# Kernel optimization log

Hardware: AMD Instinct MI355X
Metric: run time of the kernel (lower is better)

Reference implementation:

```python
import jax, jax.numpy as jnp
import numpy as np

OUT_H = OUT_W = 7
SCALE = 1.0 / 16.0
E = 256
HEADS = 8
DH = E // HEADS
ROI_GRID = 14          # scaled roi side (fixed by construction -> static shapes)
N_ROIS = 512
FH, FW = 152, 256
NQ = OUT_H * OUT_W     # 49 content queries
S = ROI_GRID * ROI_GRID  # 196 keys per roi


def setup_inputs() -> dict:
    key = jax.random.key(0)
    ks = jax.random.split(key, 8)
    features = jax.random.normal(ks[0], (1, E, FH, FW), jnp.float32)
    # rois [N,5] = (batch_idx, x1, y1, x2, y2) in image coords; side 224 px so
    # the rounded scaled grid is exactly 14x14 for every roi.
    side = ROI_GRID / SCALE  # 224.0
    x1 = jax.random.uniform(ks[1], (N_ROIS,), minval=0.0, maxval=FW / SCALE - side)
    y1 = jax.random.uniform(ks[2], (N_ROIS,), minval=0.0, maxval=FH / SCALE - side)
    rois = jnp.stack([jnp.zeros(N_ROIS), x1, y1, x1 + side, y1 + side], axis=1)
    content_queries = jax.random.normal(ks[3], (NQ, E), jnp.float32) * 0.02
    in_proj_weight = jax.random.normal(ks[4], (3 * E, E), jnp.float32) / np.sqrt(E)
    in_proj_bias = jnp.zeros((3 * E,), jnp.float32)
    out_proj_weight = jax.random.normal(ks[5], (E, E), jnp.float32) / np.sqrt(E)
    out_proj_bias = jnp.zeros((E,), jnp.float32)
    balance_param = jnp.asarray(0.0, jnp.float32)  # hardsigmoid -> 0.5
    return dict(features=features, rois=rois, content_queries=content_queries,
                in_proj_weight=in_proj_weight, in_proj_bias=in_proj_bias,
                out_proj_weight=out_proj_weight, out_proj_bias=out_proj_bias,
                balance_param=balance_param)


def _bilinear(fmap, y, x):
    """torchvision roi_align bilinear sampling. fmap [C,H,W]; y,x flat [S]."""
    C, H, W = fmap.shape
    valid = ((y >= -1.0) & (y <= H) & (x >= -1.0) & (x <= W)).astype(fmap.dtype)
    y = jnp.clip(y, 0.0, H - 1.0)
    x = jnp.clip(x, 0.0, W - 1.0)
    y0 = jnp.floor(y); x0 = jnp.floor(x)
    y0i = y0.astype(jnp.int32); x0i = x0.astype(jnp.int32)
    y1i = jnp.minimum(y0i + 1, H - 1); x1i = jnp.minimum(x0i + 1, W - 1)
    ly = y - y0; lx = x - x0; hy = 1.0 - ly; hx = 1.0 - lx
    f = lambda yi, xi: fmap[:, yi, xi]  # [C, S]
    val = (hy * hx) * f(y0i, x0i) + (hy * lx) * f(y0i, x1i) \
        + (ly * hx) * f(y1i, x0i) + (ly * lx) * f(y1i, x1i)
    return val * valid


def _roi_align(fmap, roi4, out_h, out_w, scale, sr):
    """aligned=True RoIAlign for one roi, static sampling ratio sr."""
    x1, y1, x2, y2 = roi4
    sx = x1 * scale - 0.5
    sy = y1 * scale - 0.5
    bw = (x2 - x1) * scale / out_w
    bh = (y2 - y1) * scale / out_h
    offs = (jnp.arange(sr, dtype=fmap.dtype) + 0.5) / sr
    ys = sy + (jnp.arange(out_h, dtype=fmap.dtype)[:, None] + offs[None, :]) * bh  # [out_h,sr]
    xs = sx + (jnp.arange(out_w, dtype=fmap.dtype)[:, None] + offs[None, :]) * bw  # [out_w,sr]
    Y = jnp.broadcast_to(ys[:, :, None, None], (out_h, sr, out_w, sr)).reshape(-1)
    X = jnp.broadcast_to(xs[None, None, :, :], (out_h, sr, out_w, sr)).reshape(-1)
    vals = _bilinear(fmap, Y, X)  # [C, out_h*sr*out_w*sr]
    C = fmap.shape[0]
    return vals.reshape(C, out_h, sr, out_w, sr).mean(axis=(2, 4))  # [C,out_h,out_w]


def reference(features, rois, content_queries, in_proj_weight, in_proj_bias,
              out_proj_weight, out_proj_bias, balance_param):
    fmap = features[0]                       # single image batch
    roi4 = rois[:, 1:]                       # boxes in image coords
    balance = jnp.clip(balance_param / 6.0 + 0.5, 0.0, 1.0)  # hardsigmoid(_balance)

    # position pool: RoIAlign(7x7, spatial_scale, sampling_ratio=-1 -> 2, aligned)
    pos = jax.vmap(lambda r: _roi_align(fmap, r, OUT_H, OUT_W, SCALE, 2))(roi4)
    pos = pos * balance                      # [N, C, 7, 7]

    # per-roi content pool on scaled rois at scale 1.0, grid 14x14, sr=1
    sroi = roi4 * SCALE
    cf = jax.vmap(lambda r: _roi_align(fmap, r, ROI_GRID, ROI_GRID, 1.0, 1))(sroi)
    cf = cf.reshape(N_ROIS, E, S).transpose(0, 2, 1)  # [N, S, E] (flatten(2).permute)

    # nn.MultiheadAttention(E, HEADS): shared queries, per-roi keys/values
    Wq, Wk, Wv = jnp.split(in_proj_weight, 3, axis=0)
    bq, bk, bv = jnp.split(in_proj_bias, 3, axis=0)
    q = (content_queries @ Wq.T + bq).reshape(NQ, HEADS, DH).transpose(1, 0, 2)  # [h,Q,d]
    k = (cf @ Wk.T + bk).reshape(N_ROIS, S, HEADS, DH)
    v = (cf @ Wv.T + bv).reshape(N_ROIS, S, HEADS, DH)
    logits = jnp.einsum('hqd,nshd->nhqs', q, k) / np.sqrt(DH).astype(np.float32)
    attn = jax.nn.softmax(logits, axis=-1)                     # [N,h,Q,S]
    o = jnp.einsum('nhqs,nshd->nqhd', attn, v).reshape(N_ROIS, NQ, E)
    o = o @ out_proj_weight.T + out_proj_bias                  # [N, Q, E]
    att = o.transpose(0, 2, 1).reshape(N_ROIS, E, OUT_H, OUT_W)  # .T.reshape per roi

    return pos + att * (1.0 - balance)
```

## Files before the change

kernel.cpp:

```cpp
#include <hip/hip_runtime.h>
#include <stdint.h>

#define E_DIM 256
#define HEADS 8
#define NQ 49
#define S_TOT 196
#define NROIS 512
#define FH 152
#define FW 256
#define HW_TOT (FH*FW)

typedef unsigned short u16;
typedef short bf16x8 __attribute__((ext_vector_type(8)));
typedef float f32x4 __attribute__((ext_vector_type(4)));
typedef unsigned short us8 __attribute__((ext_vector_type(8)));

#define MFMA(a,b,c) __builtin_amdgcn_mfma_f32_16x16x32_bf16((a),(b),(c),0,0,0)

__device__ __forceinline__ u16 f2bf(float f) {
  union { float f; uint32_t u; } v; v.f = f;
  uint32_t u = v.u;
  return (u16)((u + 0x7FFFu + ((u >> 16) & 1u)) >> 16);
}
__device__ __forceinline__ float bf2f(u16 h) {
  union { uint32_t u; float f; } v; v.u = ((uint32_t)h) << 16;
  return v.f;
}
__device__ __forceinline__ uint32_t cvtpk(float lo, float hi) {
  uint32_t r;
  asm("v_cvt_pk_bf16_f32 %0, %1, %2" : "=v"(r) : "v"(lo), "v"(hi));
  return r;
}
__device__ __forceinline__ bf16x8 ld_frag(const u16* p) {
  union { uint2 d[2]; bf16x8 v; } t;
  t.d[0] = *(const uint2*)(p);
  t.d[1] = *(const uint2*)(p + 4);
  return t.v;
}
__device__ __forceinline__ bf16x8 ld_frag_g(const u16* p) {
  union { uint4 d; bf16x8 v; } t;
  t.d = *(const uint4*)(p);
  return t.v;
}
__device__ __forceinline__ void gll16(const u16* g, u16* l) {
  __builtin_amdgcn_global_load_lds(
      (__attribute__((address_space(1))) void*)(g),
      (__attribute__((address_space(3))) void*)(l), 16, 0, 0);
}
__device__ __forceinline__ void win_stencil(const u16* win, int p00, int hf,
                                            float w00, float w01, float w10, float w11,
                                            float o[16]) {
  const int cA = ((hf << 1)*225) << 3;
  const int cB = cA + (225 << 3);
  const int q0 = p00 << 3;
  us8 a00 = *(const us8*)(win + cA + q0);
  us8 a01 = *(const us8*)(win + cA + q0 + 8);
  us8 a10 = *(const us8*)(win + cA + q0 + 120);
  us8 a11 = *(const us8*)(win + cA + q0 + 128);
  us8 b00 = *(const us8*)(win + cB + q0);
  us8 b01 = *(const us8*)(win + cB + q0 + 8);
  us8 b10 = *(const us8*)(win + cB + q0 + 120);
  us8 b11 = *(const us8*)(win + cB + q0 + 128);
#pragma unroll
  for (int c = 0; c < 8; ++c) {
    o[c]     = w00*bf2f(a00[c]) + w01*bf2f(a01[c]) + w10*bf2f(a10[c]) + w11*bf2f(a11[c]);
    o[c + 8] = w00*bf2f(b00[c]) + w01*bf2f(b01[c]) + w10*bf2f(b10[c]) + w11*bf2f(b11[c]);
  }
}

__global__ __launch_bounds__(256) void prep_small(
    const float* __restrict__ ipw, const float* __restrict__ opw,
    const float* __restrict__ ipb, const float* __restrict__ cq,
    u16* __restrict__ Wk, u16* __restrict__ Wv, u16* __restrict__ Wo,
    u16* __restrict__ qs)
{
  const int b = blockIdx.x;
  const int t = threadIdx.x;
  if (b < 256) {
    int i = (b << 8) + t;
    Wk[i] = f2bf(ipw[65536 + i]);
    Wv[i] = f2bf(ipw[131072 + i]);
    Wo[i] = f2bf(opw[i]);
  } else {
    const int idx = b - 256;
    const int h = idx >> 3;
    const int qq = ((idx & 7) << 3) + (t >> 5);
    const int d = t & 31;
    float acc = 0.f;
    if (qq < NQ) {
      const float4* wr = (const float4*)(ipw + (size_t)(h*32 + d)*256);
      const float4* cr = (const float4*)(cq + (size_t)qq*256);
      float s0 = 0.f, s1 = 0.f, s2 = 0.f, s3 = 0.f;
#pragma unroll
      for (int e = 0; e < 64; e += 4) {
        float4 a0 = cr[e],     b0 = wr[e];
        float4 a1 = cr[e + 1], b1 = wr[e + 1];
        float4 a2 = cr[e + 2], b2 = wr[e + 2];
        float4 a3 = cr[e + 3], b3 = wr[e + 3];
        s0 += a0.x*b0.x + a0.y*b0.y + a0.z*b0.z + a0.w*b0.w;
        s1 += a1.x*b1.x + a1.y*b1.y + a1.z*b1.z + a1.w*b1.w;
        s2 += a2.x*b2.x + a2.y*b2.y + a2.z*b2.z + a2.w*b2.w;
        s3 += a3.x*b3.x + a3.y*b3.y + a3.z*b3.z + a3.w*b3.w;
      }
      acc = (ipb[h*32 + d] + ((s0 + s1) + (s2 + s3))) * 0.17677669529663687f;
    }
    qs[h*2048 + qq*32 + d] = f2bf(acc);
  }
}

#define AT_ST 268
#define CT_ST 268
__global__ __launch_bounds__(512, 2) void proj_kv(
    const float* __restrict__ f, const u16* __restrict__ Wk, const u16* __restrict__ Wv,
    u16* __restrict__ fT, u16* __restrict__ fK, u16* __restrict__ fV)
{
  __shared__ union __align__(16) {
    u16 At[64][AT_ST];
    u16 ct[2][64][CT_ST];
  } sm;
  const int m0 = blockIdx.x << 6;
  const int t = threadIdx.x;
  const int lane = t & 63;
  const int w = t >> 6;
  const int g = lane >> 4, l15 = lane & 15;

  const int cp = t >> 4;
  const int hwq = (t & 15) << 2;
#pragma unroll
  for (int it = 0; it < 4; ++it) {
    int c = (it << 6) + (cp << 1);
    float4 v0 = *(const float4*)(f + (size_t)c*HW_TOT + m0 + hwq);
    float4 v1 = *(const float4*)(f + (size_t)(c + 1)*HW_TOT + m0 + hwq);
    *(uint32_t*)(&sm.At[hwq    ][c]) = cvtpk(v0.x, v1.x);
    *(uint32_t*)(&sm.At[hwq + 1][c]) = cvtpk(v0.y, v1.y);
    *(uint32_t*)(&sm.At[hwq + 2][c]) = cvtpk(v0.z, v1.z);
    *(uint32_t*)(&sm.At[hwq + 3][c]) = cvtpk(v0.w, v1.w);
  }
  __syncthreads();

  {
    int r = t >> 3, c0 = (t & 7) << 5;
    u16* dst = fT + (size_t)(m0 + r)*256 + c0;
#pragma unroll
    for (int k = 0; k < 4; ++k)
      *(us8*)(dst + (k << 3)) = *(const us8*)(&sm.At[r][c0 + (k << 3)]);
  }

  const int map = w >> 2;
  const u16* W = map ? Wv : Wk;
  const int nq = (w & 3) << 6;
  f32x4 acc[4][4];
#pragma unroll
  for (int mf = 0; mf < 4; ++mf)
#pragma unroll
    for (int nt = 0; nt < 4; ++nt) acc[mf][nt] = (f32x4){0.f,0.f,0.f,0.f};

#pragma unroll
  for (int kt = 0; kt < 8; ++kt) {
    bf16x8 a[4], bb[4];
#pragma unroll
    for (int mf = 0; mf < 4; ++mf)
      a[mf] = ld_frag(&sm.At[(mf << 4) + l15][(kt << 5) + (g << 3)]);
#pragma unroll
    for (int nt = 0; nt < 4; ++nt)
      bb[nt] = ld_frag_g(W + (size_t)(nq + (nt << 4) + l15)*256 + (kt << 5) + (g << 3));
#pragma unroll
    for (int mf = 0; mf < 4; ++mf)
#pragma unroll
      for (int nt = 0; nt < 4; ++nt)
        acc[mf][nt] = MFMA(a[mf], bb[nt], acc[mf][nt]);
  }
  __syncthreads();
#pragma unroll
  for (int mf = 0; mf < 4; ++mf)
#pragma unroll
    for (int nt = 0; nt < 4; ++nt)
#pragma unroll
      for (int i = 0; i < 4; ++i)
        sm.ct[map][(mf << 4) + (g << 2) + i][nq + (nt << 4) + l15] = f2bf(acc[mf][nt][i]);
  __syncthreads();
  const int map2 = w >> 2;
  u16* dstmap = map2 ? fV : fK;
#pragma unroll
  for (int hh = 0; hh < 2; ++hh) {
    int hsel = ((w & 3) << 1) + hh;
#pragma unroll
    for (int mi = 0; mi < 4; ++mi) {
      int m = (lane >> 2) + (mi << 4);
      int chunk = lane & 3;
      bf16x8 val = ld_frag(&sm.ct[map2][m][(hsel << 5) + (chunk << 3)]);
      u16* dst = dstmap + (((size_t)hsel*HW_TOT + m0 + m) << 5) + (chunk << 3);
      *(us8*)dst = *(const us8*)&val;
    }
  }
}

#define AT2_ST 228
#define KS_ST 36
#define VT_ST 228
#define OR_ST 36
#define AS_ST 260
#define PS_ST 260
struct SMemA {
  u16 attn[64][AT2_ST];
  u16 ksmp[208][KS_ST];
  u16 vT[32][VT_ST];
  u16 ore[64][OR_ST];
  u16 kwin[8192];
};
struct SMemC {
  u16 ast[NQ][AS_ST];
  u16 pos[NQ][PS_ST];
};
union __align__(16) SMem { SMemA a; SMemC c; };

__global__ __launch_bounds__(512, 4) void fused_roi_attn(
    const float* __restrict__ rois,
    const float* __restrict__ balance_p,
    const float* __restrict__ bv,
    const float* __restrict__ bout,
    const u16*  __restrict__ fT,
    const u16*  __restrict__ fK,
    const u16*  __restrict__ fV,
    const u16*  __restrict__ Woutbf,
    const u16*  __restrict__ qsPad,
    float* __restrict__ out)
{
  __shared__ SMem sm;
  u16* vwin = &sm.a.attn[0][0];
  const int tid = threadIdx.x;
  const int lane = tid & 63;
  const int w = tid >> 6;
  const int v = w >> 2;
  const int w2 = w & 3;
  const int g = lane >> 4;
  const int l15 = lane & 15;
  const int n = blockIdx.x;

  float X = rois[n*5 + 1] * 0.0625f;
  float Y = rois[n*5 + 2] * 0.0625f;
  float fx0 = floorf(X), fy0 = floorf(Y);
  const int ix0 = (int)fx0, iy0 = (int)fy0;
  const float lx = X - fx0, ly = Y - fy0;
  const float hx = 1.0f - lx, hy = 1.0f - ly;
  const float w00 = hy*hx, w01 = hy*lx, w10 = ly*hx, w11 = ly*lx;

  int srcoff[2];
#pragma unroll
  for (int i = 0; i < 2; ++i) {
    int u = (w << 7) + (i << 6) + lane;
    int uc = min(u, 899);
    int c = uc / 225;
    int p = uc - c*225;
    int pr = p / 15, pc2 = p - pr*15;
    int yg = min(iy0 + pr, FH - 1);
    int xg = min(ix0 + pc2, FW - 1);
    srcoff[i] = (((yg << 8) + xg) << 5) + (c << 3);
  }
  const int u0 = ((w << 7) << 3);
  const int u1 = u0 + (64 << 3);

  const int s_slot = tid & 255;
  const int hf = tid >> 8;
  const bool smp = s_slot < S_TOT;
  int p00 = 0;
  if (smp) { int gy = s_slot/14, gx = s_slot - gy*14; p00 = gy*15 + gx; }
  const int hstep = HW_TOT << 5;

  for (int i = tid; i < 32*32; i += 512) sm.a.vT[i >> 5][196 + (i & 31)] = 0;
  for (int i = tid; i < 64*16; i += 512) sm.a.attn[i >> 4][208 + (i & 15)] = 0;

  float bal;
  { float bp = balance_p[0]; bal = fminf(fmaxf(bp*(1.0f/6.0f) + 0.5f, 0.0f), 1.0f); }

  f32x4 attacc[8];
#pragma unroll
  for (int i = 0; i < 8; ++i) attacc[i] = (f32x4){0.f,0.f,0.f,0.f};

  gll16(fK + srcoff[0], sm.a.kwin + u0);
  gll16(fK + srcoff[1], sm.a.kwin + u1);

  for (int h = 0; h < HEADS; ++h) {
    __syncthreads();

    {
      const u16* fVh = fV + h*hstep;
      gll16(fVh + srcoff[0], vwin + u0);
      gll16(fVh + srcoff[1], vwin + u1);
    }
    if (smp) {
      float kk[16];
      win_stencil(sm.a.kwin, p00, hf, w00, w01, w10, w11, kk);
      u16* krow = &sm.a.ksmp[s_slot][hf << 4];
      uint2 q0 = {cvtpk(kk[0],kk[1]),   cvtpk(kk[2],kk[3])};
      uint2 q1 = {cvtpk(kk[4],kk[5]),   cvtpk(kk[6],kk[7])};
      uint2 q2 = {cvtpk(kk[8],kk[9]),   cvtpk(kk[10],kk[11])};
      uint2 q3 = {cvtpk(kk[12],kk[13]), cvtpk(kk[14],kk[15])};
      *(uint2*)(krow)      = q0;
      *(uint2*)(krow + 4)  = q1;
      *(uint2*)(krow + 8)  = q2;
      *(uint2*)(krow + 12) = q3;
    }
    __syncthreads();

    if (smp) {
      float vv[16];
      win_stencil(vwin, p00, hf, w00, w01, w10, w11, vv);
#pragma unroll
      for (int j = 0; j < 16; j += 2) {
        uint32_t p = cvtpk(vv[j], vv[j+1]);
        sm.a.vT[(hf << 4) + j][s_slot]     = (u16)p;
        sm.a.vT[(hf << 4) + j + 1][s_slot] = (u16)(p >> 16);
      }
    }
    __syncthreads();

    if (h + 1 < HEADS) {
      const u16* fKh = fK + (h+1)*hstep;
      gll16(fKh + srcoff[0], sm.a.kwin + u0);
      gll16(fKh + srcoff[1], sm.a.kwin + u1);
    }

    __builtin_amdgcn_s_setprio(1);

    bf16x8 aq = ld_frag_g(qsPad + (size_t)((h << 6) + (w2 << 4) + l15)*32 + (g << 3));
    float sum[4] = {0.f, 0.f, 0.f, 0.f};
#pragma unroll
    for (int nt = 0; nt < 13; ++nt) {
      bf16x8 bk = ld_frag(&sm.a.ksmp[(nt << 4) + l15][g << 3]);
      f32x4 z = (f32x4){0.f,0.f,0.f,0.f};
      f32x4 lg = MFMA(aq, bk, z);
#pragma unroll
      for (int i = 0; i < 4; ++i) {
        float p = (nt == 12 && l15 >= 4) ? 0.f : __expf(fminf(lg[i], 80.f));
        sum[i] += p;
        sm.a.attn[(w2 << 4) + (g << 2) + i][(nt << 4) + l15] = f2bf(p);
      }
    }
    float srow[4];
#pragma unroll
    for (int i = 0; i < 4; ++i) {
#pragma unroll
      for (int off = 1; off < 16; off <<= 1) sum[i] += __shfl_xor(sum[i], off, 64);
      srow[i] = 1.0f / sum[i];
    }

    f32x4 o0 = (f32x4){0.f,0.f,0.f,0.f}, o1 = (f32x4){0.f,0.f,0.f,0.f};
#pragma unroll
    for (int kt = 0; kt < 7; ++kt) {
      bf16x8 ap = ld_frag(&sm.a.attn[(w2 << 4) + l15][(kt << 5) + (g << 3)]);
      bf16x8 b0 = ld_frag(&sm.a.vT[l15][(kt << 5) + (g << 3)]);
      bf16x8 b1 = ld_frag(&sm.a.vT[16 + l15][(kt << 5) + (g << 3)]);
      o0 = MFMA(ap, b0, o0);
      o1 = MFMA(ap, b1, o1);
    }
    float bv0 = bv[(h << 5) + l15];
    float bv1 = bv[(h << 5) + 16 + l15];
#pragma unroll
    for (int i = 0; i < 4; ++i) {
      sm.a.ore[(w2 << 4) + (g << 2) + i][l15]      = f2bf(o0[i]*srow[i] + bv0);
      sm.a.ore[(w2 << 4) + (g << 2) + i][16 + l15] = f2bf(o1[i]*srow[i] + bv1);
    }
    bf16x8 ao = ld_frag(&sm.a.ore[(w2 << 4) + l15][g << 3]);
#pragma unroll
    for (int j = 0; j < 8; ++j) {
      int nt = (v << 3) + j;
      bf16x8 bo = ld_frag_g(Woutbf + (size_t)((nt << 4) + l15)*256 + (h << 5) + (g << 3));
      attacc[j] = MFMA(ao, bo, attacc[j]);
    }
    __builtin_amdgcn_s_setprio(0);
  }

  __syncthreads();
#pragma unroll
  for (int j = 0; j < 8; ++j) {
    int nt = (v << 3) + j;
    float bo = bout[(nt << 4) + l15];
#pragma unroll
    for (int i = 0; i < 4; ++i) {
      int r = (w2 << 4) + (g << 2) + i;
      if (r < NQ) sm.c.ast[r][(nt << 4) + l15] = f2bf(attacc[j][i] + bo);
    }
  }
  {
    float wy[3] = {hy, 1.0f, ly};
    float wx[3] = {hx, 1.0f, lx};
    for (int it = 0; it < 4; ++it) {
      int item = tid + (it << 9);
      if (item < NQ*32) {
        int q = item >> 5, c8 = (item & 31) << 3;
        int oy = q/7, ox = q - oy*7;
        float a[8] = {0.f,0.f,0.f,0.f,0.f,0.f,0.f,0.f};
#pragma unroll
        for (int j = 0; j < 3; ++j) {
          int ry = min(iy0 + (oy << 1) + j, FH - 1);
#pragma unroll
          for (int i = 0; i < 3; ++i) {
            int rx = min(ix0 + (ox << 1) + i, FW - 1);
            const u16* pt = fT + (((size_t)(ry*FW + rx)) << 8) + c8;
            us8 tv = *(const us8*)pt;
            float wji = wy[j]*wx[i];
#pragma unroll
            for (int c = 0; c < 8; ++c) a[c] += wji*bf2f(tv[c]);
          }
        }
        uint2 r0 = {cvtpk(0.25f*a[0], 0.25f*a[1]), cvtpk(0.25f*a[2], 0.25f*a[3])};
        uint2 r1 = {cvtpk(0.25f*a[4], 0.25f*a[5]), cvtpk(0.25f*a[6], 0.25f*a[7])};
        *(uint2*)(&sm.c.pos[q][c8])     = r0;
        *(uint2*)(&sm.c.pos[q][c8 + 4]) = r1;
      }
    }
  }
  __syncthreads();
  float ibal = 1.0f - bal;
  float* outp = out + (size_t)n*(E_DIM*NQ);
  for (int j = 0; j < 25; ++j) {
    int idx = (j << 9) + tid;
    if (idx < E_DIM*NQ) {
      int eo = idx/49;
      int q  = idx - eo*49;
      outp[idx] = bal*bf2f(sm.c.pos[q][eo]) + ibal*bf2f(sm.c.ast[q][eo]);
    }
  }
}

extern "C" void kernel_launch(void* const* d_in, const int* in_sizes, int n_in,
                              void* d_out, int out_size, void* d_ws, size_t ws_size,
                              hipStream_t stream) {
  const float* features = (const float*)d_in[0];
  const float* rois     = (const float*)d_in[1];
  const float* cq       = (const float*)d_in[2];
  const float* ipw      = (const float*)d_in[3];
  const float* ipb      = (const float*)d_in[4];
  const float* opw      = (const float*)d_in[5];
  const float* opb      = (const float*)d_in[6];
  const float* balp     = (const float*)d_in[7];
  float* out = (float*)d_out;

  char* ws = (char*)d_ws;
  const size_t FMB = (size_t)HW_TOT*256*2;
  u16* fT = (u16*)ws;
  u16* fK = (u16*)(ws + FMB);
  u16* fV = (u16*)(ws + 2*FMB);
  u16* Wk = (u16*)(ws + 3*FMB);
  u16* Wv = Wk + 65536;
  u16* Wo = Wv + 65536;
  u16* qs = Wo + 65536;

  hipLaunchKernelGGL(prep_small, dim3(320), dim3(256), 0, stream,
                     ipw, opw, ipb, cq, Wk, Wv, Wo, qs);
  hipLaunchKernelGGL(proj_kv,    dim3(HW_TOT/64), dim3(512), 0, stream,
                     features, Wk, Wv, fT, fK, fV);
  hipLaunchKernelGGL(fused_roi_attn, dim3(NROIS), dim3(512), 0, stream,
                     rois, balp, ipb + 512, opb, fT, fK, fV, Wo, qs, out);
}
```

Measured before the change: 132.0 us.

## Fold K bilinear weights into scaled queries and prefetch K/V windows together

Drops the explicit K sampling stencil and its shared-memory staging buffer. The query fragment is scaled by each of the four bilinear weights, and logits are built with four accumulated MFMAs that read the raw K window directly. V now gets its own shared-memory window, so the K and V windows for the next head are both prefetched together after the V stencil, and one barrier per head is removed. This quadruples the QK MFMA count and LDS fragment reads in exchange for less VALU stencil work and less synchronisation. It also rounds the weight-scaled queries to bf16, which slightly changes numerics.

```diff
diff --git a/kernel.cpp b/kernel.cpp
--- a/kernel.cpp
+++ b/kernel.cpp
@@ -66,6 +66,14 @@
     o[c]     = w00*bf2f(a00[c]) + w01*bf2f(a01[c]) + w10*bf2f(a10[c]) + w11*bf2f(a11[c]);
     o[c + 8] = w00*bf2f(b00[c]) + w01*bf2f(b01[c]) + w10*bf2f(b10[c]) + w11*bf2f(b11[c]);
   }
+}
+__device__ __forceinline__ bf16x8 scale_q(const float a8[8], float wp) {
+  union { uint4 d; bf16x8 v; } t;
+  t.d.x = cvtpk(a8[0]*wp, a8[1]*wp);
+  t.d.y = cvtpk(a8[2]*wp, a8[3]*wp);
+  t.d.z = cvtpk(a8[4]*wp, a8[5]*wp);
+  t.d.w = cvtpk(a8[6]*wp, a8[7]*wp);
+  return t.v;
 }
 
 __global__ __launch_bounds__(256) void prep_small(
@@ -196,17 +204,17 @@
 }
 
 #define AT2_ST 228
-#define KS_ST 36
 #define VT_ST 228
 #define OR_ST 36
 #define AS_ST 260
 #define PS_ST 260
+#define WIN_U16 7680
 struct SMemA {
   u16 attn[64][AT2_ST];
-  u16 ksmp[208][KS_ST];
   u16 vT[32][VT_ST];
   u16 ore[64][OR_ST];
-  u16 kwin[8192];
+  u16 kwin[WIN_U16];
+  u16 vwin[WIN_U16];
 };
 struct SMemC {
   u16 ast[NQ][AS_ST];
@@ -227,7 +235,6 @@
     float* __restrict__ out)
 {
   __shared__ SMem sm;
-  u16* vwin = &sm.a.attn[0][0];
   const int tid = threadIdx.x;
   const int lane = tid & 63;
   const int w = tid >> 6;
@@ -257,8 +264,9 @@
     int xg = min(ix0 + pc2, FW - 1);
     srcoff[i] = (((yg << 8) + xg) << 5) + (c << 3);
   }
-  const int u0 = ((w << 7) << 3);
-  const int u1 = u0 + (64 << 3);
+  const int u0 = (w << 7) << 3;
+  const int u1 = u0 + 512;
+  const bool wv7 = (w < 7);
 
   const int s_slot = tid & 255;
   const int hf = tid >> 8;
@@ -278,34 +286,57 @@
   for (int i = 0; i < 8; ++i) attacc[i] = (f32x4){0.f,0.f,0.f,0.f};
 
   gll16(fK + srcoff[0], sm.a.kwin + u0);
-  gll16(fK + srcoff[1], sm.a.kwin + u1);
+  if (wv7) gll16(fK + srcoff[1], sm.a.kwin + u1);
+  gll16(fV + srcoff[0], sm.a.vwin + u0);
+  if (wv7) gll16(fV + srcoff[1], sm.a.vwin + u1);
 
   for (int h = 0; h < HEADS; ++h) {
     __syncthreads();
 
-    {
-      const u16* fVh = fV + h*hstep;
-      gll16(fVh + srcoff[0], vwin + u0);
-      gll16(fVh + srcoff[1], vwin + u1);
-    }
-    if (smp) {
-      float kk[16];
-      win_stencil(sm.a.kwin, p00, hf, w00, w01, w10, w11, kk);
-      u16* krow = &sm.a.ksmp[s_slot][hf << 4];
-      uint2 q0 = {cvtpk(kk[0],kk[1]),   cvtpk(kk[2],kk[3])};
-      uint2 q1 = {cvtpk(kk[4],kk[5]),   cvtpk(kk[6],kk[7])};
-      uint2 q2 = {cvtpk(kk[8],kk[9]),   cvtpk(kk[10],kk[11])};
-      uint2 q3 = {cvtpk(kk[12],kk[13]), cvtpk(kk[14],kk[15])};
-      *(uint2*)(krow)      = q0;
-      *(uint2*)(krow + 4)  = q1;
-      *(uint2*)(krow + 8)  = q2;
-      *(uint2*)(krow + 12) = q3;
-    }
-    __syncthreads();
+    __builtin_amdgcn_s_setprio(1);
+    bf16x8 aqr = ld_frag_g(qsPad + (size_t)((h << 6) + (w2 << 4) + l15)*32 + (g << 3));
+    float a8[8];
+#pragma unroll
+    for (int c = 0; c < 8; ++c) a8[c] = bf2f((u16)aqr[c]);
+    bf16x8 aq00 = scale_q(a8, w00);
+    bf16x8 aq01 = scale_q(a8, w01);
+    bf16x8 aq10 = scale_q(a8, w10);
+    bf16x8 aq11 = scale_q(a8, w11);
+
+    float sum[4] = {0.f, 0.f, 0.f, 0.f};
+#pragma unroll
+    for (int nt = 0; nt < 13; ++nt) {
+      int s = (nt << 4) + l15;
+      int gy = s / 14;
+      const u16* kp = sm.a.kwin + ((g*225 + s + gy) << 3);
+      bf16x8 b00 = ld_frag(kp);
+      bf16x8 b01 = ld_frag(kp + 8);
+      bf16x8 b10 = ld_frag(kp + 120);
+      bf16x8 b11 = ld_frag(kp + 128);
+      f32x4 z = (f32x4){0.f,0.f,0.f,0.f};
+      f32x4 lg = MFMA(aq00, b00, z);
+      lg = MFMA(aq01, b01, lg);
+      lg = MFMA(aq10, b10, lg);
+      lg = MFMA(aq11, b11, lg);
+#pragma unroll
+      for (int i = 0; i < 4; ++i) {
+        float p = (nt == 12 && l15 >= 4) ? 0.f : __expf(fminf(lg[i], 80.f));
+        sum[i] += p;
+        sm.a.attn[(w2 << 4) + (g << 2) + i][(nt << 4) + l15] = f2bf(p);
+      }
+    }
+    float srow[4];
+#pragma unroll
+    for (int i = 0; i < 4; ++i) {
+#pragma unroll
+      for (int off = 1; off < 16; off <<= 1) sum[i] += __shfl_xor(sum[i], off, 64);
+      srow[i] = 1.0f / sum[i];
+    }
+    __builtin_amdgcn_s_setprio(0);
 
     if (smp) {
       float vv[16];
-      win_stencil(vwin, p00, hf, w00, w01, w10, w11, vv);
+      win_stencil(sm.a.vwin, p00, hf, w00, w01, w10, w11, vv);
 #pragma unroll
       for (int j = 0; j < 16; j += 2) {
         uint32_t p = cvtpk(vv[j], vv[j+1]);
@@ -317,34 +348,14 @@
 
     if (h + 1 < HEADS) {
       const u16* fKh = fK + (h+1)*hstep;
+      const u16* fVh = fV + (h+1)*hstep;
       gll16(fKh + srcoff[0], sm.a.kwin + u0);
-      gll16(fKh + srcoff[1], sm.a.kwin + u1);
+      if (wv7) gll16(fKh + srcoff[1], sm.a.kwin + u1);
+      gll16(fVh + srcoff[0], sm.a.vwin + u0);
+      if (wv7) gll16(fVh + srcoff[1], sm.a.vwin + u1);
     }
 
     __builtin_amdgcn_s_setprio(1);
-
-    bf16x8 aq = ld_frag_g(qsPad + (size_t)((h << 6) + (w2 << 4) + l15)*32 + (g << 3));
-    float sum[4] = {0.f, 0.f, 0.f, 0.f};
-#pragma unroll
-    for (int nt = 0; nt < 13; ++nt) {
-      bf16x8 bk = ld_frag(&sm.a.ksmp[(nt << 4) + l15][g << 3]);
-      f32x4 z = (f32x4){0.f,0.f,0.f,0.f};
-      f32x4 lg = MFMA(aq, bk, z);
-#pragma unroll
-      for (int i = 0; i < 4; ++i) {
-        float p = (nt == 12 && l15 >= 4) ? 0.f : __expf(fminf(lg[i], 80.f));
-        sum[i] += p;
-        sm.a.attn[(w2 << 4) + (g << 2) + i][(nt << 4) + l15] = f2bf(p);
-      }
-    }
-    float srow[4];
-#pragma unroll
-    for (int i = 0; i < 4; ++i) {
-#pragma unroll
-      for (int off = 1; off < 16; off <<= 1) sum[i] += __shfl_xor(sum[i], off, 64);
-      srow[i] = 1.0f / sum[i];
-    }
-
     f32x4 o0 = (f32x4){0.f,0.f,0.f,0.f}, o1 = (f32x4){0.f,0.f,0.f,0.f};
 #pragma unroll
     for (int kt = 0; kt < 7; ++kt) {
```

Measured after the change: 144.6 us. +9.5%, slower.

## Shrink proj_kv tiles to 16 pixels per block for higher occupancy

Applied to the files above, without the earlier changes.

Restructures the K/V projection kernel so each block handles 16 spatial positions with 256 threads instead of 64 positions with 512 threads, launching four times as many blocks with a smaller LDS footprint and fewer accumulators per wave. The aim is more resident waves and better latency hiding on the feature-map loads. In exchange, weight fragments from global memory are reused across only one 16-row M fragment instead of four, so weight reads from global/L2 roughly quadruple per output.

```diff
diff --git a/kernel.cpp b/kernel.cpp
--- a/kernel.cpp
+++ b/kernel.cpp
@@ -109,89 +109,76 @@
 }
 
 #define AT_ST 268
-#define CT_ST 268
-__global__ __launch_bounds__(512, 2) void proj_kv(
+__global__ __launch_bounds__(256, 8) void proj_kv(
     const float* __restrict__ f, const u16* __restrict__ Wk, const u16* __restrict__ Wv,
     u16* __restrict__ fT, u16* __restrict__ fK, u16* __restrict__ fV)
 {
   __shared__ union __align__(16) {
-    u16 At[64][AT_ST];
-    u16 ct[2][64][CT_ST];
+    u16 At[16][AT_ST];
+    u16 ct[2][16][AT_ST];
   } sm;
-  const int m0 = blockIdx.x << 6;
+  const int m0 = blockIdx.x << 4;
   const int t = threadIdx.x;
   const int lane = t & 63;
   const int w = t >> 6;
   const int g = lane >> 4, l15 = lane & 15;
-
-  const int cp = t >> 4;
-  const int hwq = (t & 15) << 2;
-#pragma unroll
-  for (int it = 0; it < 4; ++it) {
-    int c = (it << 6) + (cp << 1);
-    float4 v0 = *(const float4*)(f + (size_t)c*HW_TOT + m0 + hwq);
-    float4 v1 = *(const float4*)(f + (size_t)(c + 1)*HW_TOT + m0 + hwq);
-    *(uint32_t*)(&sm.At[hwq    ][c]) = cvtpk(v0.x, v1.x);
-    *(uint32_t*)(&sm.At[hwq + 1][c]) = cvtpk(v0.y, v1.y);
-    *(uint32_t*)(&sm.At[hwq + 2][c]) = cvtpk(v0.z, v1.z);
-    *(uint32_t*)(&sm.At[hwq + 3][c]) = cvtpk(v0.w, v1.w);
+  const int map = w >> 1;
+  const int nh = w & 1;
+  const u16* W = map ? Wv : Wk;
+
+  {
+    const int cpq = t >> 2;
+    const int hwq = (t & 3) << 2;
+#pragma unroll
+    for (int it = 0; it < 2; ++it) {
+      int c = (((it << 6) + cpq) << 1);
+      float4 v0 = *(const float4*)(f + (size_t)c*HW_TOT + m0 + hwq);
+      float4 v1 = *(const float4*)(f + (size_t)(c + 1)*HW_TOT + m0 + hwq);
+      *(uint32_t*)(&sm.At[hwq    ][c]) = cvtpk(v0.x, v1.x);
+      *(uint32_t*)(&sm.At[hwq + 1][c]) = cvtpk(v0.y, v1.y);
+      *(uint32_t*)(&sm.At[hwq + 2][c]) = cvtpk(v0.z, v1.z);
+      *(uint32_t*)(&sm.At[hwq + 3][c]) = cvtpk(v0.w, v1.w);
+    }
   }
   __syncthreads();
 
   {
-    int r = t >> 3, c0 = (t & 7) << 5;
+    int r = t >> 4, c0 = (t & 15) << 4;
     u16* dst = fT + (size_t)(m0 + r)*256 + c0;
-#pragma unroll
-    for (int k = 0; k < 4; ++k)
-      *(us8*)(dst + (k << 3)) = *(const us8*)(&sm.At[r][c0 + (k << 3)]);
-  }
-
-  const int map = w >> 2;
-  const u16* W = map ? Wv : Wk;
-  const int nq = (w & 3) << 6;
-  f32x4 acc[4][4];
-#pragma unroll
-  for (int mf = 0; mf < 4; ++mf)
-#pragma unroll
-    for (int nt = 0; nt < 4; ++nt) acc[mf][nt] = (f32x4){0.f,0.f,0.f,0.f};
+    *(us8*)(dst)     = *(const us8*)(&sm.At[r][c0]);
+    *(us8*)(dst + 8) = *(const us8*)(&sm.At[r][c0 + 8]);
+  }
+
+  f32x4 acc[8];
+#pragma unroll
+  for (int nt = 0; nt < 8; ++nt) acc[nt] = (f32x4){0.f,0.f,0.f,0.f};
 
 #pragma unroll
   for (int kt = 0; kt < 8; ++kt) {
-    bf16x8 a[4], bb[4];
-#pragma unroll
-    for (int mf = 0; mf < 4; ++mf)
-      a[mf] = ld_frag(&sm.At[(mf << 4) + l15][(kt << 5) + (g << 3)]);
-#pragma unroll
-    for (int nt = 0; nt < 4; ++nt)
-      bb[nt] = ld_frag_g(W + (size_t)(nq + (nt << 4) + l15)*256 + (kt << 5) + (g << 3));
-#pragma unroll
-    for (int mf = 0; mf < 4; ++mf)
-#pragma unroll
-      for (int nt = 0; nt < 4; ++nt)
-        acc[mf][nt] = MFMA(a[mf], bb[nt], acc[mf][nt]);
+    bf16x8 a = ld_frag(&sm.At[l15][(kt << 5) + (g << 3)]);
+#pragma unroll
+    for (int nt = 0; nt < 8; ++nt) {
+      bf16x8 bb = ld_frag_g(W + (size_t)((nh << 7) + (nt << 4) + l15)*256 + (kt << 5) + (g << 3));
+      acc[nt] = MFMA(a, bb, acc[nt]);
+    }
   }
   __syncthreads();
 #pragma unroll
-  for (int mf = 0; mf < 4; ++mf)
-#pragma unroll
-    for (int nt = 0; nt < 4; ++nt)
-#pragma unroll
-      for (int i = 0; i < 4; ++i)
-        sm.ct[map][(mf << 4) + (g << 2) + i][nq + (nt << 4) + l15] = f2bf(acc[mf][nt][i]);
+  for (int nt = 0; nt < 8; ++nt)
+#pragma unroll
+    for (int i = 0; i < 4; ++i)
+      sm.ct[map][(g << 2) + i][(nh << 7) + (nt << 4) + l15] = f2bf(acc[nt][i]);
   __syncthreads();
-  const int map2 = w >> 2;
-  u16* dstmap = map2 ? fV : fK;
-#pragma unroll
-  for (int hh = 0; hh < 2; ++hh) {
-    int hsel = ((w & 3) << 1) + hh;
-#pragma unroll
-    for (int mi = 0; mi < 4; ++mi) {
-      int m = (lane >> 2) + (mi << 4);
-      int chunk = lane & 3;
-      bf16x8 val = ld_frag(&sm.ct[map2][m][(hsel << 5) + (chunk << 3)]);
-      u16* dst = dstmap + (((size_t)hsel*HW_TOT + m0 + m) << 5) + (chunk << 3);
-      *(us8*)dst = *(const us8*)&val;
-    }
+  {
+    const int map2 = t >> 7;
+    const int tt = t & 127;
+    const int hsel = tt >> 4;
+    const int r2 = tt & 15;
+    u16* dst = (map2 ? fV : fK) + (((size_t)hsel*HW_TOT + m0 + r2) << 5);
+    const u16* srcp = &sm.ct[map2][r2][hsel << 5];
+#pragma unroll
+    for (int chunk = 0; chunk < 4; ++chunk)
+      *(us8*)(dst + (chunk << 3)) = *(const us8*)(srcp + (chunk << 3));
   }
 }
 
@@ -449,7 +436,7 @@
 
   hipLaunchKernelGGL(prep_small, dim3(320), dim3(256), 0, stream,
                      ipw, opw, ipb, cq, Wk, Wv, Wo, qs);
-  hipLaunchKernelGGL(proj_kv,    dim3(HW_TOT/64), dim3(512), 0, stream,
+  hipLaunchKernelGGL(proj_kv,    dim3(HW_TOT/16), dim3(256), 0, stream,
                      features, Wk, Wv, fT, fK, fV);
   hipLaunchKernelGGL(fused_roi_attn, dim3(NROIS), dim3(512), 0, stream,
                      rois, balp, ipb + 512, opb, fT, fK, fV, Wo, qs, out);
```

Result: slower. 208.9 us (+58.2%).
